# Optimization experiments

Hardware: AMD Instinct MI355X
Metric: run time of the kernel (lower is better)

Reference implementation:

```python
import jax, jax.numpy as jnp
import numpy as np

B, P, L, H = 64, 1024, 16, 256
NUM_SIZE = 18
TOPK = min(64, P)


def _ramp(epoch, a, b):
    if epoch <= a:
        return 0.0
    if epoch >= b:
        return 1.0
    return float(epoch - a) / float(b - a)


def _normalize(x):
    return x / jnp.maximum(jnp.linalg.norm(x, axis=-1, keepdims=True), 1e-12)


def setup_inputs() -> dict:
    key = jax.random.key(0)
    ks = jax.random.split(key, 16)
    return {
        'pred_center': jax.random.normal(ks[0], (B, P, 3), dtype=jnp.float32),
        'pred_size': jax.random.uniform(ks[1], (B, P, 3), minval=0.2, maxval=1.0, dtype=jnp.float32),
        'bbox_feature': jax.random.normal(ks[2], (B, P, H), dtype=jnp.float32),
        'objectness_scores': jax.random.normal(ks[3], (B, P, 2), dtype=jnp.float32),
        'lang_emb': jax.random.normal(ks[4], (B * L, H), dtype=jnp.float32),
        'lang_num': jax.random.randint(ks[5], (B,), 1, L + 1),
        'ref_center': jax.random.normal(ks[6], (B, L, 3), dtype=jnp.float32),
        'ref_size_class': jax.random.randint(ks[7], (B, L), 0, NUM_SIZE),
        'ref_size_residual': jax.random.uniform(ks[8], (B, L, 3), minval=0.0, maxval=0.2, dtype=jnp.float32),
        'mean_size_arr': jax.random.uniform(ks[9], (NUM_SIZE, 3), minval=0.3, maxval=1.5, dtype=jnp.float32),
        'W_text': jax.random.normal(ks[10], (H, H), dtype=jnp.float32) / np.sqrt(H),
        'W_pc': jax.random.normal(ks[11], (H, H), dtype=jnp.float32) / np.sqrt(H),
        'W_pc_iou': jax.random.normal(ks[12], (H, H), dtype=jnp.float32) / np.sqrt(H),
        'log_inv_tau': jnp.array([np.log(1.0 / 0.07)], dtype=jnp.float32),
        'epoch': 40,
    }


def _forward(pred_center, pred_size, bbox_feature, objectness_scores, lang_emb,
             lang_num, ref_center, ref_size_class, ref_size_residual,
             mean_size_arr, W_text, W_pc, W_pc_iou, log_inv_tau, epoch):
    b, l = ref_center.shape[:2]
    # curriculum (python scalars, epoch is a static int)
    p = _ramp(epoch, 0, 80)
    thr = 0.05 + 0.3 * p
    gamma = 1.0 + 2.0 * p
    min_tau = 0.08 - 0.04 * p

    # top-k proposals by objectness prob
    obj_prob = jax.nn.softmax(objectness_scores, axis=2)[..., 1]  # (B,P)
    _, topk_inds = jax.lax.top_k(obj_prob, TOPK)                  # (B,K)
    feat = jnp.take_along_axis(bbox_feature, topk_inds[..., None], axis=1)  # (B,K,H)
    ctr = jnp.take_along_axis(pred_center, topk_inds[..., None], axis=1)    # (B,K,3)
    sz = jnp.take_along_axis(pred_size, topk_inds[..., None], axis=1)       # (B,K,3)

    # axis-aligned 3D IoU between gt boxes (B,L) and pred boxes (B,K) -- detached
    gt_size = mean_size_arr[ref_size_class] + ref_size_residual + 0.01  # (B,L,3)
    gmin, gmax = ref_center - gt_size / 2, ref_center + gt_size / 2
    pmin, pmax = ctr - sz / 2, ctr + sz / 2
    lo = jnp.maximum(gmin[:, :, None], pmin[:, None])   # (B,L,K,3)
    hi = jnp.minimum(gmax[:, :, None], pmax[:, None])
    inter = jnp.prod(jnp.clip(hi - lo, 0.0, None), axis=-1)  # (B,L,K)
    vol_g = jnp.prod(gt_size, axis=-1)[:, :, None]
    vol_p = jnp.prod(sz, axis=-1)[:, None]
    iou = jax.lax.stop_gradient(inter / (vol_g + vol_p - inter + 1e-7))  # (B,L,K)

    # soft target over proposals (detached)
    w = jnp.clip(iou, 0.0, None) ** gamma * (iou >= thr).astype(iou.dtype)
    onehot = jax.nn.one_hot(jnp.argmax(iou, axis=-1), TOPK, dtype=iou.dtype)
    w = jnp.where(w.sum(-1, keepdims=True) < 1e-6, onehot, w)
    target = w / (w.sum(-1, keepdims=True) + 1e-6)  # (B,L,K)

    # temperature
    inv_tau = jnp.minimum(jnp.exp(log_inv_tau)[0], 100.0)
    inv_tau = jnp.minimum(inv_tau, 1.0 / max(min_tau, 1e-6))

    # language-box contrastive
    text = _normalize(lang_emb.reshape(b, l, -1) @ W_text.T)  # (B,L,H)
    boxf = _normalize(feat @ W_pc.T)                          # (B,K,H)
    sim = jnp.einsum('blh,bkh->blk', text, boxf)              # (B,L,K)
    logp = jax.nn.log_softmax(sim * inv_tau, axis=-1)
    t2 = target / (target.sum(-1, keepdims=True) + 1e-6)      # soft_ce renorm
    ce = -(t2 * logp).sum(-1)                                 # (B,L)

    neg = iou < 0.05
    s_neg = jnp.max(jnp.where(neg, sim, -jnp.inf), axis=-1)
    s_pos = (sim * target).sum(-1)
    rank = jnp.where(neg.any(-1), jax.nn.relu(0.2 - s_pos + s_neg), 0.0)
    lang_con = ce + 0.5 * rank                                # (B,L)

    mask = (jnp.arange(l)[None, :] < lang_num[:, None]).astype(sim.dtype)
    lang_loss = (lang_con * mask).sum() / b

    # iou-aware box-box contrastive
    tm = w[..., :, None] * w[..., None, :]                    # (B,L,K,K) detached
    tm = tm / (tm.sum(-1, keepdims=True) + 1e-6)
    tm = tm / (tm.sum(-1, keepdims=True) + 1e-6)              # soft_ce renorm
    boxf_iou = _normalize(feat @ W_pc_iou.T)                  # (B,K,H)
    sim_iou = jnp.einsum('bkh,bmh->bkm', boxf_iou, boxf_iou)  # (B,K,K)
    logp_iou = jax.nn.log_softmax(sim_iou * inv_tau, axis=-1)
    iou_ce = -(tm * logp_iou[:, None]).sum(-1).mean(-1)       # (B,L)
    iou_loss = (iou_ce * mask).sum() / b

    return jnp.stack([lang_loss, iou_loss])


def reference(pred_center, pred_size, bbox_feature, objectness_scores, lang_emb,
              lang_num, ref_center, ref_size_class, ref_size_residual,
              mean_size_arr, W_text, W_pc, W_pc_iou, log_inv_tau, epoch):
    return _forward(pred_center, pred_size, bbox_feature, objectness_scores,
                    lang_emb, lang_num, ref_center, ref_size_class,
                    ref_size_residual, mean_size_arr, W_text, W_pc, W_pc_iou,
                    log_inv_tau, epoch)
```

## Files before the change

kernel.cpp:

```cpp
#include <hip/hip_runtime.h>
#include <math.h>

#define B 64
#define P 1024
#define L 16
#define H 256
#define K 64

__device__ __forceinline__ float wsum(float v){
  #pragma unroll
  for (int o = 32; o >= 1; o >>= 1) v += __shfl_xor(v, o, 64);
  return v;
}
__device__ __forceinline__ float wmaxr(float v){
  #pragma unroll
  for (int o = 32; o >= 1; o >>= 1) v = fmaxf(v, __shfl_xor(v, o, 64));
  return v;
}
__device__ __forceinline__ void wargmax(float &v, int &i){
  #pragma unroll
  for (int o = 32; o >= 1; o >>= 1){
    float v2 = __shfl_xor(v, o, 64);
    int   i2 = __shfl_xor(i, o, 64);
    if (v2 > v || (v2 == v && i2 < i)){ v = v2; i = i2; }
  }
}
__device__ __forceinline__ unsigned fkey(float f){
  unsigned b = __float_as_uint(f);
  return (b & 0x80000000u) ? ~b : (b | 0x80000000u);
}
__device__ __forceinline__ float dot4(float4 a, float4 b){
  return a.x*b.x + a.y*b.y + a.z*b.z + a.w*b.w;
}
__device__ __forceinline__ int gsw(int r){ return (r ^ (r >> 3)) & 7; }

__global__ __launch_bounds__(256) void k_topk_iou(
    const float* __restrict__ pred_center, const float* __restrict__ pred_size,
    const float* __restrict__ obj, const float* __restrict__ ref_center,
    const int* __restrict__ ref_cls, const float* __restrict__ ref_res,
    const float* __restrict__ mean_sz, const int* __restrict__ epoch_p,
    const int* __restrict__ lang_num,
    int* __restrict__ inds, float* __restrict__ iou_ws, float* __restrict__ w_ws,
    float* __restrict__ c_ws, float* __restrict__ t_ws, float* __restrict__ t2_ws,
    float* __restrict__ t2s_ws, int* __restrict__ cnt)
{
  __shared__ int hist[256];
  __shared__ int s_digit, s_cum;
  __shared__ int waveTot[4];
  __shared__ int sel[K];
  __shared__ float ctrS[K][3], szS[K][3];
  int b = blockIdx.x, tid = threadIdx.x, lane = tid & 63, wave = tid >> 6;
  if (b == 0 && tid == 0) *cnt = 0;

  const float4* o4 = (const float4*)(obj + (size_t)b*P*2);
  float4 va = o4[tid*2], vb = o4[tid*2+1];
  unsigned kj[4] = { fkey(va.y - va.x), fkey(va.w - va.z),
                     fkey(vb.y - vb.x), fkey(vb.w - vb.z) };

  unsigned prefix = 0; int rem = K;
  for (int pass = 0; pass < 4; ++pass){
    int shift = 24 - pass*8;
    hist[tid] = 0;
    __syncthreads();
    #pragma unroll
    for (int j = 0; j < 4; ++j){
      unsigned kk = kj[j];
      bool cand = (pass == 0) || ((kk >> (shift + 8)) == prefix);
      if (cand) atomicAdd(&hist[(kk >> shift) & 0xff], 1);
    }
    __syncthreads();
    int d = 255 - tid;
    int h = hist[d];
    int s = h;
    #pragma unroll
    for (int o = 1; o < 64; o <<= 1){ int t = __shfl_up(s, o, 64); if (lane >= o) s += t; }
    if (lane == 63) waveTot[wave] = s;
    __syncthreads();
    #pragma unroll
    for (int q = 0; q < 3; ++q) if (q < wave) s += waveTot[q];
    if (s >= rem && s - h < rem){ s_digit = d; s_cum = s - h; }
    __syncthreads();
    prefix = (prefix << 8) | (unsigned)s_digit;
    rem -= s_cum;
    __syncthreads();
  }
  unsigned T = prefix;
  int remFinal = rem;

  int eqc = 0;
  #pragma unroll
  for (int j = 0; j < 4; ++j) eqc += (kj[j] == T) ? 1 : 0;
  int v = eqc;
  #pragma unroll
  for (int o = 1; o < 64; o <<= 1){ int t = __shfl_up(v, o, 64); if (lane >= o) v += t; }
  if (lane == 63) waveTot[wave] = v;
  __syncthreads();
  int off = 0;
  for (int q = 0; q < wave; ++q) off += waveTot[q];
  int e = off + v - eqc;
  __syncthreads();

  int selc = 0; bool ch[4];
  #pragma unroll
  for (int j = 0; j < 4; ++j){
    bool g = kj[j] > T;
    bool q = (kj[j] == T) && (e < remFinal);
    if (kj[j] == T) e++;
    ch[j] = g || q; selc += ch[j] ? 1 : 0;
  }
  v = selc;
  #pragma unroll
  for (int o = 1; o < 64; o <<= 1){ int t = __shfl_up(v, o, 64); if (lane >= o) v += t; }
  if (lane == 63) waveTot[wave] = v;
  __syncthreads();
  off = 0;
  for (int q = 0; q < wave; ++q) off += waveTot[q];
  int slot = off + v - selc;
  #pragma unroll
  for (int j = 0; j < 4; ++j) if (ch[j]) sel[slot++] = tid*4 + j;
  __syncthreads();

  if (tid < K){
    int idx = sel[tid];
    inds[b*K + tid] = idx;
    #pragma unroll
    for (int dd = 0; dd < 3; ++dd){
      ctrS[tid][dd] = pred_center[((size_t)b*P + idx)*3 + dd];
      szS [tid][dd] = pred_size [((size_t)b*P + idx)*3 + dd];
    }
  }
  __syncthreads();

  int ep = epoch_p[0];
  float pr = ep <= 0 ? 0.f : (ep >= 80 ? 1.f : ep / 80.f);
  float thr = 0.05f + 0.3f * pr;
  float gamma = 1.f + 2.f * pr;
  int ln = lang_num[b];

  for (int l = wave; l < L; l += 4){
    int cls = ref_cls[b*L + l];
    float gs[3], gc[3]; float volg = 1.f;
    #pragma unroll
    for (int dd = 0; dd < 3; ++dd){
      gs[dd] = mean_sz[cls*3+dd] + ref_res[((size_t)b*L+l)*3+dd] + 0.01f;
      gc[dd] = ref_center[((size_t)b*L+l)*3+dd];
      volg *= gs[dd];
    }
    int k = lane;
    float inter = 1.f, volp = 1.f;
    #pragma unroll
    for (int dd = 0; dd < 3; ++dd){
      float pc = ctrS[k][dd], ps = szS[k][dd];
      float lo = fmaxf(gc[dd]-gs[dd]*0.5f, pc-ps*0.5f);
      float hi = fminf(gc[dd]+gs[dd]*0.5f, pc+ps*0.5f);
      inter *= fmaxf(hi-lo, 0.f);
      volp *= ps;
    }
    float iou = inter / (volg + volp - inter + 1e-7f);
    float wv = (iou >= thr) ? powf(iou, gamma) : 0.f;
    float S = wsum(wv);
    float av = iou; int ai = k;
    wargmax(av, ai);
    float wfin = (S < 1e-6f) ? ((k == ai) ? 1.f : 0.f) : wv;
    iou_ws[((size_t)b*L + l)*K + k] = iou;
    w_ws  [((size_t)b*L + l)*K + k] = wfin;
    float Sf = (S < 1e-6f) ? 1.f : S;
    float a = wfin * Sf;
    float c = wfin / ((a + 1e-6f) * (a/(a + 1e-6f) + 1e-6f));
    c_ws[((size_t)b*L + l)*K + k] = (l < ln) ? c : 0.f;
    float target = wfin / (Sf + 1e-6f);
    float tsum = Sf / (Sf + 1e-6f);
    float t2 = target / (tsum + 1e-6f);
    t_ws [((size_t)b*L + l)*K + k] = target;
    t2_ws[((size_t)b*L + l)*K + k] = t2;
    float T2S = wsum(t2);
    if (lane == 0) t2s_ws[b*L + l] = T2S;
  }
}

__global__ __launch_bounds__(256) void k_gemm(
    const float* __restrict__ bbox_feature, const int* __restrict__ inds,
    const float* __restrict__ lang_emb,
    const float* __restrict__ Wpc, const float* __restrict__ Wpci,
    const float* __restrict__ Wtext,
    float* __restrict__ boxr, float* __restrict__ boxri, float* __restrict__ texr)
{
  __shared__ float As[2][32][68], Ws[2][32][68];
  int gb = blockIdx.x;
  const float *W; float *C; int m0; bool gat;
  if (gb < 64)       { W = Wpc;   C = boxr;  m0 = gb*64;       gat = true;  }
  else if (gb < 128) { W = Wpci;  C = boxri; m0 = (gb-64)*64;  gat = true;  }
  else               { W = Wtext; C = texr;  m0 = (gb-128)*64; gat = false; }
  int bcol = blockIdx.y * 64;
  int tid = threadIdx.x;
  int lr = tid >> 2, lc = (tid & 3) * 4;
  int tr = tid >> 4, tc = tid & 15;
  int r = m0 + lr;
  const float* Arow = gat ? bbox_feature + ((size_t)(r >> 6)*P + inds[r])*H
                          : lang_emb + (size_t)r*H;
  const float* Wrow = W + (size_t)(bcol + lr)*H;
  float acc[4][4] = {};

  {
    float4 av  = *(const float4*)&Arow[lc];
    float4 av2 = *(const float4*)&Arow[16 + lc];
    float4 wv  = *(const float4*)&Wrow[lc];
    float4 wv2 = *(const float4*)&Wrow[16 + lc];
    As[0][lc+0][lr]=av.x;  As[0][lc+1][lr]=av.y;  As[0][lc+2][lr]=av.z;  As[0][lc+3][lr]=av.w;
    As[0][16+lc+0][lr]=av2.x; As[0][16+lc+1][lr]=av2.y; As[0][16+lc+2][lr]=av2.z; As[0][16+lc+3][lr]=av2.w;
    Ws[0][lc+0][lr]=wv.x;  Ws[0][lc+1][lr]=wv.y;  Ws[0][lc+2][lr]=wv.z;  Ws[0][lc+3][lr]=wv.w;
    Ws[0][16+lc+0][lr]=wv2.x; Ws[0][16+lc+1][lr]=wv2.y; Ws[0][16+lc+2][lr]=wv2.z; Ws[0][16+lc+3][lr]=wv2.w;
  }
  __syncthreads();

  int cur = 0;
  for (int h0 = 0; h0 < H; h0 += 32){
    float4 av, av2, wv, wv2;
    bool pre = (h0 + 32 < H);
    if (pre){
      av  = *(const float4*)&Arow[h0 + 32 + lc];
      av2 = *(const float4*)&Arow[h0 + 48 + lc];
      wv  = *(const float4*)&Wrow[h0 + 32 + lc];
      wv2 = *(const float4*)&Wrow[h0 + 48 + lc];
    }
    #pragma unroll
    for (int h = 0; h < 32; ++h){
      float4 a = *(const float4*)&As[cur][h][tr*4];
      float4 w = *(const float4*)&Ws[cur][h][tc*4];
      float aa[4] = {a.x,a.y,a.z,a.w};
      float ww[4] = {w.x,w.y,w.z,w.w};
      #pragma unroll
      for (int i = 0; i < 4; ++i)
        #pragma unroll
        for (int j = 0; j < 4; ++j) acc[i][j] += aa[i]*ww[j];
    }
    if (pre){
      int nx = cur ^ 1;
      As[nx][lc+0][lr]=av.x;  As[nx][lc+1][lr]=av.y;  As[nx][lc+2][lr]=av.z;  As[nx][lc+3][lr]=av.w;
      As[nx][16+lc+0][lr]=av2.x; As[nx][16+lc+1][lr]=av2.y; As[nx][16+lc+2][lr]=av2.z; As[nx][16+lc+3][lr]=av2.w;
      Ws[nx][lc+0][lr]=wv.x;  Ws[nx][lc+1][lr]=wv.y;  Ws[nx][lc+2][lr]=wv.z;  Ws[nx][lc+3][lr]=wv.w;
      Ws[nx][16+lc+0][lr]=wv2.x; Ws[nx][16+lc+1][lr]=wv2.y; Ws[nx][16+lc+2][lr]=wv2.z; Ws[nx][16+lc+3][lr]=wv2.w;
      __syncthreads();
      cur = nx;
    }
  }
  #pragma unroll
  for (int i = 0; i < 4; ++i){
    float4 v = make_float4(acc[i][0],acc[i][1],acc[i][2],acc[i][3]);
    *(float4*)&C[(size_t)(m0+tr*4+i)*H + bcol + tc*4] = v;
  }
}

__global__ __launch_bounds__(512) void k_contrast(
    const float* __restrict__ texr, const float* __restrict__ boxr,
    const float* __restrict__ boxri,
    const float* __restrict__ iou_ws, const float* __restrict__ w_ws,
    const float* __restrict__ c_ws, const float* __restrict__ t_ws,
    const float* __restrict__ t2_ws, const float* __restrict__ t2s_ws,
    const int* __restrict__ lang_num, const float* __restrict__ log_inv_tau,
    const int* __restrict__ epoch_p, float* __restrict__ part,
    int* __restrict__ cnt, float* __restrict__ out)
{
  extern __shared__ __align__(16) float smem[];
  __shared__ float redI[8], redL[8];
  __shared__ int s_done;
  int tid = threadIdx.x, lane = tid & 63, wave = tid >> 6;
  int ep = epoch_p[0];
  float pr = ep <= 0 ? 0.f : (ep >= 80 ? 1.f : ep / 80.f);
  float min_tau = fmaxf(0.08f - 0.04f*pr, 1e-6f);
  float itau = fminf(fminf(expf(log_inv_tau[0]), 100.f), 1.f/min_tau);

  if (blockIdx.x < 64){
    int b = blockIdx.x;
    float4* TB = (float4*)smem;
    float4* TT = (float4*)smem + 4096;
    const float4* srcB = (const float4*)(boxr + (size_t)b*K*H);
    const float4* srcT = (const float4*)(texr + (size_t)b*L*H);
    #pragma unroll
    for (int j = 0; j < 8; ++j){
      int i4 = tid + 512*j;
      int row = i4 >> 6, c = i4 & 63;
      TB[row*64 + (c ^ gsw(row))] = srcB[i4];
    }
    #pragma unroll
    for (int j = 0; j < 2; ++j){
      int i4 = tid + 512*j;
      int row = i4 >> 6, c = i4 & 63;
      TT[row*64 + (c ^ gsw(row))] = srcT[i4];
    }
    __syncthreads();

    int l0 = wave*2;
    float acc[2] = {0,0}, nt2[2] = {0,0};
    float nb2 = 0.f;
    for (int c = 0; c < 64; ++c){
      float4 bx = TB[lane*64 + (c ^ gsw(lane))];
      nb2 += dot4(bx, bx);
      #pragma unroll
      for (int i = 0; i < 2; ++i){
        int l = l0 + i;
        float4 tv = TT[l*64 + (c ^ gsw(l))];
        acc[i] += dot4(tv, bx);
        nt2[i] += dot4(tv, tv);
      }
    }
    float nb = fmaxf(sqrtf(nb2), 1e-12f);
    int ln = lang_num[b];
    float bacc = 0.f;
    #pragma unroll
    for (int i = 0; i < 2; ++i){
      int l = l0 + i;
      if (l < ln){
        float sv = acc[i] / (fmaxf(sqrtf(nt2[i]), 1e-12f) * nb);
        float target = t_ws [((size_t)b*L + l)*K + lane];
        float t2     = t2_ws[((size_t)b*L + l)*K + lane];
        float iou    = iou_ws[((size_t)b*L + l)*K + lane];
        float T2S    = t2s_ws[b*L + l];
        float z = sv * itau;
        float zmax = wmaxr(z);
        float se = wsum(expf(z - zmax));
        float t2z = wsum(t2 * z);
        float ce = -t2z + (zmax + logf(se)) * T2S;
        bool neg = iou < 0.05f;
        float sneg = wmaxr(neg ? sv : -INFINITY);
        int anyneg = __any(neg);
        float spos = wsum(sv * target);
        float rank = anyneg ? fmaxf(0.2f - spos + sneg, 0.f) : 0.f;
        bacc += ce + 0.5f*rank;
      }
    }
    if (lane == 0) atomicExch(&part[blockIdx.x*8 + wave], bacc);
  } else {
    int idx = blockIdx.x - 64;
    int b = idx >> 1, half = idx & 1;
    int r0 = half*32 + wave*4;
    float4* TI = (float4*)smem;
    float*  cL = smem + 16384;
    const float4* srcI = (const float4*)(boxri + (size_t)b*K*H);
    #pragma unroll
    for (int j = 0; j < 8; ++j){
      int i4 = tid + 512*j;
      int row = i4 >> 6, c = i4 & 63;
      TI[row*64 + (c ^ gsw(row))] = srcI[i4];
    }
    {
      int l = tid >> 5, kk = tid & 31;
      cL[l*32 + kk] = c_ws[((size_t)b*L + l)*K + half*32 + kk];
    }
    float wl[16];
    #pragma unroll
    for (int l = 0; l < 16; ++l) wl[l] = w_ws[((size_t)b*L + l)*K + lane];
    __syncthreads();

    float acc[4] = {0,0,0,0};
    float nm2 = 0.f;
    for (int c = 0; c < 64; ++c){
      float4 bx = TI[lane*64 + (c ^ gsw(lane))];
      nm2 += dot4(bx, bx);
      #pragma unroll
      for (int i = 0; i < 4; ++i){
        float4 kq = TI[(r0+i)*64 + (c ^ gsw(r0+i))];
        acc[i] += dot4(kq, bx);
      }
    }
    float4 Mv = make_float4(0.f,0.f,0.f,0.f);
    #pragma unroll
    for (int l = 0; l < 16; ++l){
      float4 cq = *(const float4*)&cL[l*32 + wave*4];
      Mv.x += cq.x * wl[l]; Mv.y += cq.y * wl[l];
      Mv.z += cq.z * wl[l]; Mv.w += cq.w * wl[l];
    }
    float Ma[4] = {Mv.x, Mv.y, Mv.z, Mv.w};
    float nm = fmaxf(sqrtf(nm2), 1e-12f);
    float contrib = 0.f;
    #pragma unroll
    for (int i = 0; i < 4; ++i){
      float nk = __shfl(nm, r0 + i, 64);
      float sv = acc[i] / (nk * nm);
      float z = sv * itau;
      float zmax = wmaxr(z);
      float se = wsum(expf(z - zmax));
      float lp = z - zmax - logf(se);
      contrib += Ma[i] * lp;
    }
    float bacc = -wsum(contrib) * (1.f/64.f);
    if (lane == 0) atomicExch(&part[512 + idx*8 + wave], bacc);
  }

  __syncthreads();
  if (tid == 0){
    __threadfence();
    int t = atomicAdd(cnt, 1);
    s_done = (t == 191) ? 1 : 0;
  }
  __syncthreads();
  if (s_done){
    float vl = atomicAdd(&part[tid], 0.f);
    float vi = atomicAdd(&part[512 + tid], 0.f)
             + atomicAdd(&part[1024 + tid], 0.f);
    vi = wsum(vi);
    vl = wsum(vl);
    if (lane == 0){ redI[wave] = vi; redL[wave] = vl; }
    __syncthreads();
    if (tid == 0){
      float sl = 0.f, si = 0.f;
      #pragma unroll
      for (int q = 0; q < 8; ++q){ sl += redL[q]; si += redI[q]; }
      out[0] = sl * (1.f/64.f);
      out[1] = si * (1.f/64.f);
    }
  }
}

extern "C" void kernel_launch(void* const* d_in, const int* in_sizes, int n_in,
                              void* d_out, int out_size, void* d_ws, size_t ws_size,
                              hipStream_t stream)
{
  const float* pred_center = (const float*)d_in[0];
  const float* pred_size   = (const float*)d_in[1];
  const float* bbox_feature= (const float*)d_in[2];
  const float* obj         = (const float*)d_in[3];
  const float* lang_emb    = (const float*)d_in[4];
  const int*   lang_num    = (const int*)d_in[5];
  const float* ref_center  = (const float*)d_in[6];
  const int*   ref_cls     = (const int*)d_in[7];
  const float* ref_res     = (const float*)d_in[8];
  const float* mean_sz     = (const float*)d_in[9];
  const float* Wtext       = (const float*)d_in[10];
  const float* Wpc         = (const float*)d_in[11];
  const float* Wpci        = (const float*)d_in[12];
  const float* lit         = (const float*)d_in[13];
  const int*   epoch       = (const int*)d_in[14];

  float* ws = (float*)d_ws;
  int*   inds   = (int*)ws;
  float* iou_ws = ws + 4096;
  float* w_ws   = iou_ws + B*L*K;
  float* c_ws   = w_ws + B*L*K;
  float* t_ws   = c_ws + B*L*K;
  float* t2_ws  = t_ws + B*L*K;
  float* t2s_ws = t2_ws + B*L*K;
  float* texr   = t2s_ws + B*L;
  float* boxr   = texr + (size_t)B*L*H;
  float* boxri  = boxr + (size_t)B*K*H;
  float* part   = boxri + (size_t)B*K*H;
  int*   cnt    = (int*)(part + 1536);

  k_topk_iou<<<B, 256, 0, stream>>>(pred_center, pred_size, obj, ref_center,
                                    ref_cls, ref_res, mean_sz, epoch, lang_num,
                                    inds, iou_ws, w_ws, c_ws, t_ws, t2_ws, t2s_ws,
                                    cnt);
  k_gemm<<<dim3(144, 4), 256, 0, stream>>>(bbox_feature, inds, lang_emb,
                                           Wpc, Wpci, Wtext, boxr, boxri, texr);
  k_contrast<<<192, 512, 81920, stream>>>(texr, boxr, boxri,
                                          iou_ws, w_ws, c_ws, t_ws, t2_ws, t2s_ws,
                                          lang_num, lit, epoch, part, cnt,
                                          (float*)d_out);
}
```

Measured before the change: 58.90 us.

## Rewrite projection GEMM as one-wave blocks with 8x8 register tiles

The gather+projection GEMM is restructured so each 64-thread block computes a 64x64 output tile, with every thread holding an 8x8 accumulator instead of 4x4. The grid is flattened to 576 blocks, and the double-buffered shared-memory pipeline is replaced by a single buffer with two barriers per 32-wide K slice. The aim is more register-level reuse per shared-memory load, at the cost of fewer waves per block, higher register pressure and no overlap between global loads and compute.

```diff
diff --git a/kernel.cpp b/kernel.cpp
--- a/kernel.cpp
+++ b/kernel.cpp
@@ -178,76 +178,63 @@
   }
 }
 
-__global__ __launch_bounds__(256) void k_gemm(
+__global__ __launch_bounds__(64) void k_gemm(
     const float* __restrict__ bbox_feature, const int* __restrict__ inds,
     const float* __restrict__ lang_emb,
     const float* __restrict__ Wpc, const float* __restrict__ Wpci,
     const float* __restrict__ Wtext,
     float* __restrict__ boxr, float* __restrict__ boxri, float* __restrict__ texr)
 {
-  __shared__ float As[2][32][68], Ws[2][32][68];
+  __shared__ float As[32][68], Ws[32][68];
   int gb = blockIdx.x;
-  const float *W; float *C; int m0; bool gat;
-  if (gb < 64)       { W = Wpc;   C = boxr;  m0 = gb*64;       gat = true;  }
-  else if (gb < 128) { W = Wpci;  C = boxri; m0 = (gb-64)*64;  gat = true;  }
-  else               { W = Wtext; C = texr;  m0 = (gb-128)*64; gat = false; }
-  int bcol = blockIdx.y * 64;
+  const float *W; float *C; int m0, bcol; bool gat;
+  if (gb < 256)      { W = Wpc;   C = boxr;  m0 = (gb>>2)*64;       bcol = (gb&3)*64; gat = true;  }
+  else if (gb < 512) { W = Wpci;  C = boxri; m0 = ((gb-256)>>2)*64; bcol = (gb&3)*64; gat = true;  }
+  else               { W = Wtext; C = texr;  m0 = ((gb-512)>>2)*64; bcol = (gb&3)*64; gat = false; }
   int tid = threadIdx.x;
-  int lr = tid >> 2, lc = (tid & 3) * 4;
-  int tr = tid >> 4, tc = tid & 15;
-  int r = m0 + lr;
-  const float* Arow = gat ? bbox_feature + ((size_t)(r >> 6)*P + inds[r])*H
-                          : lang_emb + (size_t)r*H;
-  const float* Wrow = W + (size_t)(bcol + lr)*H;
-  float acc[4][4] = {};
-
-  {
-    float4 av  = *(const float4*)&Arow[lc];
-    float4 av2 = *(const float4*)&Arow[16 + lc];
-    float4 wv  = *(const float4*)&Wrow[lc];
-    float4 wv2 = *(const float4*)&Wrow[16 + lc];
-    As[0][lc+0][lr]=av.x;  As[0][lc+1][lr]=av.y;  As[0][lc+2][lr]=av.z;  As[0][lc+3][lr]=av.w;
-    As[0][16+lc+0][lr]=av2.x; As[0][16+lc+1][lr]=av2.y; As[0][16+lc+2][lr]=av2.z; As[0][16+lc+3][lr]=av2.w;
-    Ws[0][lc+0][lr]=wv.x;  Ws[0][lc+1][lr]=wv.y;  Ws[0][lc+2][lr]=wv.z;  Ws[0][lc+3][lr]=wv.w;
-    Ws[0][16+lc+0][lr]=wv2.x; Ws[0][16+lc+1][lr]=wv2.y; Ws[0][16+lc+2][lr]=wv2.z; Ws[0][16+lc+3][lr]=wv2.w;
-  }
-  __syncthreads();
-
-  int cur = 0;
-  for (int h0 = 0; h0 < H; h0 += 32){
-    float4 av, av2, wv, wv2;
-    bool pre = (h0 + 32 < H);
-    if (pre){
-      av  = *(const float4*)&Arow[h0 + 32 + lc];
-      av2 = *(const float4*)&Arow[h0 + 48 + lc];
-      wv  = *(const float4*)&Wrow[h0 + 32 + lc];
-      wv2 = *(const float4*)&Wrow[h0 + 48 + lc];
-    }
+  int tr = tid >> 3, tc = tid & 7;
+  int sr = tid >> 3, sc = tid & 7;
+
+  float acc[8][8] = {};
+  for (int h0 = 0; h0 < 64; h0 += 8){
+    #pragma unroll
+    for (int j = 0; j < 8; ++j){
+      int row = sr + 8*j;
+      int r = m0 + row;
+      const float4* asrc = gat
+        ? (const float4*)(bbox_feature + ((size_t)(r >> 6)*P + inds[r])*H)
+        : (const float4*)(lang_emb + (size_t)r*H);
+      const float4* wsrc = (const float4*)(W + (size_t)(bcol + row)*H);
+      float4 av = asrc[h0 + sc];
+      float4 wv = wsrc[h0 + sc];
+      As[sc*4+0][row] = av.x; As[sc*4+1][row] = av.y;
+      As[sc*4+2][row] = av.z; As[sc*4+3][row] = av.w;
+      Ws[sc*4+0][row] = wv.x; Ws[sc*4+1][row] = wv.y;
+      Ws[sc*4+2][row] = wv.z; Ws[sc*4+3][row] = wv.w;
+    }
+    __syncthreads();
     #pragma unroll
     for (int h = 0; h < 32; ++h){
-      float4 a = *(const float4*)&As[cur][h][tr*4];
-      float4 w = *(const float4*)&Ws[cur][h][tc*4];
-      float aa[4] = {a.x,a.y,a.z,a.w};
-      float ww[4] = {w.x,w.y,w.z,w.w};
+      float4 a0 = *(const float4*)&As[h][tr*8];
+      float4 a1 = *(const float4*)&As[h][tr*8+4];
+      float4 w0 = *(const float4*)&Ws[h][tc*8];
+      float4 w1 = *(const float4*)&Ws[h][tc*8+4];
+      float aa[8] = {a0.x,a0.y,a0.z,a0.w,a1.x,a1.y,a1.z,a1.w};
+      float ww[8] = {w0.x,w0.y,w0.z,w0.w,w1.x,w1.y,w1.z,w1.w};
       #pragma unroll
-      for (int i = 0; i < 4; ++i)
+      for (int i = 0; i < 8; ++i)
         #pragma unroll
-        for (int j = 0; j < 4; ++j) acc[i][j] += aa[i]*ww[j];
-    }
-    if (pre){
-      int nx = cur ^ 1;
-      As[nx][lc+0][lr]=av.x;  As[nx][lc+1][lr]=av.y;  As[nx][lc+2][lr]=av.z;  As[nx][lc+3][lr]=av.w;
-      As[nx][16+lc+0][lr]=av2.x; As[nx][16+lc+1][lr]=av2.y; As[nx][16+lc+2][lr]=av2.z; As[nx][16+lc+3][lr]=av2.w;
-      Ws[nx][lc+0][lr]=wv.x;  Ws[nx][lc+1][lr]=wv.y;  Ws[nx][lc+2][lr]=wv.z;  Ws[nx][lc+3][lr]=wv.w;
-      Ws[nx][16+lc+0][lr]=wv2.x; Ws[nx][16+lc+1][lr]=wv2.y; Ws[nx][16+lc+2][lr]=wv2.z; Ws[nx][16+lc+3][lr]=wv2.w;
-      __syncthreads();
-      cur = nx;
-    }
-  }
-  #pragma unroll
-  for (int i = 0; i < 4; ++i){
-    float4 v = make_float4(acc[i][0],acc[i][1],acc[i][2],acc[i][3]);
-    *(float4*)&C[(size_t)(m0+tr*4+i)*H + bcol + tc*4] = v;
+        for (int j = 0; j < 8; ++j) acc[i][j] += aa[i]*ww[j];
+    }
+    __syncthreads();
+  }
+  #pragma unroll
+  for (int i = 0; i < 8; ++i){
+    float4 v0 = make_float4(acc[i][0],acc[i][1],acc[i][2],acc[i][3]);
+    float4 v1 = make_float4(acc[i][4],acc[i][5],acc[i][6],acc[i][7]);
+    size_t base = (size_t)(m0 + tr*8 + i)*H + bcol + tc*8;
+    *(float4*)&C[base]     = v0;
+    *(float4*)&C[base + 4] = v1;
   }
 }
 
@@ -450,8 +437,8 @@
                                     ref_cls, ref_res, mean_sz, epoch, lang_num,
                                     inds, iou_ws, w_ws, c_ws, t_ws, t2_ws, t2s_ws,
                                     cnt);
-  k_gemm<<<dim3(144, 4), 256, 0, stream>>>(bbox_feature, inds, lang_emb,
-                                           Wpc, Wpci, Wtext, boxr, boxri, texr);
+  k_gemm<<<dim3(576), 64, 0, stream>>>(bbox_feature, inds, lang_emb,
+                                       Wpc, Wpci, Wtext, boxr, boxri, texr);
   k_contrast<<<192, 512, 81920, stream>>>(texr, boxr, boxri,
                                           iou_ws, w_ws, c_ws, t_ws, t2_ws, t2s_ws,
                                           lang_num, lit, epoch, part, cnt,
```

New measurement: 88.31 us. +49.9%, slower.

## Split GEMM reduction dimension in two and sum partials in contrast kernel

Applied to the files above, without the earlier changes.

The GEMM grid gains a z dimension that splits the H=256 reduction into two halves. Each half writes its own partial output buffer, and the contrast kernel adds the two partials while loading them into shared memory. This doubles the GEMM block count (576 to 1152) to fill more compute units, and drops the register double-buffered prefetch in favour of a simpler single shared buffer. The cost is extra workspace, twice the partial-output writes, extra reads in the contrast kernel, and loads that no longer overlap with compute.

```diff
diff --git a/kernel.cpp b/kernel.cpp
--- a/kernel.cpp
+++ b/kernel.cpp
@@ -31,6 +31,9 @@
 }
 __device__ __forceinline__ float dot4(float4 a, float4 b){
   return a.x*b.x + a.y*b.y + a.z*b.z + a.w*b.w;
+}
+__device__ __forceinline__ float4 f4add(float4 a, float4 b){
+  return make_float4(a.x+b.x, a.y+b.y, a.z+b.z, a.w+b.w);
 }
 __device__ __forceinline__ int gsw(int r){ return (r ^ (r >> 3)) & 7; }
 
@@ -183,14 +186,16 @@
     const float* __restrict__ lang_emb,
     const float* __restrict__ Wpc, const float* __restrict__ Wpci,
     const float* __restrict__ Wtext,
-    float* __restrict__ boxr, float* __restrict__ boxri, float* __restrict__ texr)
+    float* __restrict__ boxr0, float* __restrict__ boxri0, float* __restrict__ texr0,
+    float* __restrict__ boxr1, float* __restrict__ boxri1, float* __restrict__ texr1)
 {
-  __shared__ float As[2][32][68], Ws[2][32][68];
+  __shared__ float As[32][68], Ws[32][68];
   int gb = blockIdx.x;
+  int z  = blockIdx.z;
   const float *W; float *C; int m0; bool gat;
-  if (gb < 64)       { W = Wpc;   C = boxr;  m0 = gb*64;       gat = true;  }
-  else if (gb < 128) { W = Wpci;  C = boxri; m0 = (gb-64)*64;  gat = true;  }
-  else               { W = Wtext; C = texr;  m0 = (gb-128)*64; gat = false; }
+  if (gb < 64)       { W = Wpc;   C = z ? boxr1  : boxr0;  m0 = gb*64;       gat = true;  }
+  else if (gb < 128) { W = Wpci;  C = z ? boxri1 : boxri0; m0 = (gb-64)*64;  gat = true;  }
+  else               { W = Wtext; C = z ? texr1  : texr0;  m0 = (gb-128)*64; gat = false; }
   int bcol = blockIdx.y * 64;
   int tid = threadIdx.x;
   int lr = tid >> 2, lc = (tid & 3) * 4;
@@ -200,33 +205,21 @@
                           : lang_emb + (size_t)r*H;
   const float* Wrow = W + (size_t)(bcol + lr)*H;
   float acc[4][4] = {};
-
-  {
-    float4 av  = *(const float4*)&Arow[lc];
-    float4 av2 = *(const float4*)&Arow[16 + lc];
-    float4 wv  = *(const float4*)&Wrow[lc];
-    float4 wv2 = *(const float4*)&Wrow[16 + lc];
-    As[0][lc+0][lr]=av.x;  As[0][lc+1][lr]=av.y;  As[0][lc+2][lr]=av.z;  As[0][lc+3][lr]=av.w;
-    As[0][16+lc+0][lr]=av2.x; As[0][16+lc+1][lr]=av2.y; As[0][16+lc+2][lr]=av2.z; As[0][16+lc+3][lr]=av2.w;
-    Ws[0][lc+0][lr]=wv.x;  Ws[0][lc+1][lr]=wv.y;  Ws[0][lc+2][lr]=wv.z;  Ws[0][lc+3][lr]=wv.w;
-    Ws[0][16+lc+0][lr]=wv2.x; Ws[0][16+lc+1][lr]=wv2.y; Ws[0][16+lc+2][lr]=wv2.z; Ws[0][16+lc+3][lr]=wv2.w;
-  }
-  __syncthreads();
-
-  int cur = 0;
-  for (int h0 = 0; h0 < H; h0 += 32){
-    float4 av, av2, wv, wv2;
-    bool pre = (h0 + 32 < H);
-    if (pre){
-      av  = *(const float4*)&Arow[h0 + 32 + lc];
-      av2 = *(const float4*)&Arow[h0 + 48 + lc];
-      wv  = *(const float4*)&Wrow[h0 + 32 + lc];
-      wv2 = *(const float4*)&Wrow[h0 + 48 + lc];
-    }
+  int hbeg = z * 128, hend = hbeg + 128;
+  for (int h0 = hbeg; h0 < hend; h0 += 32){
+    float4 av  = *(const float4*)&Arow[h0 + lc];
+    float4 av2 = *(const float4*)&Arow[h0 + 16 + lc];
+    float4 wv  = *(const float4*)&Wrow[h0 + lc];
+    float4 wv2 = *(const float4*)&Wrow[h0 + 16 + lc];
+    As[lc+0][lr]=av.x;  As[lc+1][lr]=av.y;  As[lc+2][lr]=av.z;  As[lc+3][lr]=av.w;
+    As[16+lc+0][lr]=av2.x; As[16+lc+1][lr]=av2.y; As[16+lc+2][lr]=av2.z; As[16+lc+3][lr]=av2.w;
+    Ws[lc+0][lr]=wv.x;  Ws[lc+1][lr]=wv.y;  Ws[lc+2][lr]=wv.z;  Ws[lc+3][lr]=wv.w;
+    Ws[16+lc+0][lr]=wv2.x; Ws[16+lc+1][lr]=wv2.y; Ws[16+lc+2][lr]=wv2.z; Ws[16+lc+3][lr]=wv2.w;
+    __syncthreads();
     #pragma unroll
     for (int h = 0; h < 32; ++h){
-      float4 a = *(const float4*)&As[cur][h][tr*4];
-      float4 w = *(const float4*)&Ws[cur][h][tc*4];
+      float4 a = *(const float4*)&As[h][tr*4];
+      float4 w = *(const float4*)&Ws[h][tc*4];
       float aa[4] = {a.x,a.y,a.z,a.w};
       float ww[4] = {w.x,w.y,w.z,w.w};
       #pragma unroll
@@ -234,15 +227,7 @@
         #pragma unroll
         for (int j = 0; j < 4; ++j) acc[i][j] += aa[i]*ww[j];
     }
-    if (pre){
-      int nx = cur ^ 1;
-      As[nx][lc+0][lr]=av.x;  As[nx][lc+1][lr]=av.y;  As[nx][lc+2][lr]=av.z;  As[nx][lc+3][lr]=av.w;
-      As[nx][16+lc+0][lr]=av2.x; As[nx][16+lc+1][lr]=av2.y; As[nx][16+lc+2][lr]=av2.z; As[nx][16+lc+3][lr]=av2.w;
-      Ws[nx][lc+0][lr]=wv.x;  Ws[nx][lc+1][lr]=wv.y;  Ws[nx][lc+2][lr]=wv.z;  Ws[nx][lc+3][lr]=wv.w;
-      Ws[nx][16+lc+0][lr]=wv2.x; Ws[nx][16+lc+1][lr]=wv2.y; Ws[nx][16+lc+2][lr]=wv2.z; Ws[nx][16+lc+3][lr]=wv2.w;
-      __syncthreads();
-      cur = nx;
-    }
+    __syncthreads();
   }
   #pragma unroll
   for (int i = 0; i < 4; ++i){
@@ -252,8 +237,9 @@
 }
 
 __global__ __launch_bounds__(512) void k_contrast(
-    const float* __restrict__ texr, const float* __restrict__ boxr,
-    const float* __restrict__ boxri,
+    const float* __restrict__ texr0, const float* __restrict__ texr1,
+    const float* __restrict__ boxr0, const float* __restrict__ boxr1,
+    const float* __restrict__ boxri0, const float* __restrict__ boxri1,
     const float* __restrict__ iou_ws, const float* __restrict__ w_ws,
     const float* __restrict__ c_ws, const float* __restrict__ t_ws,
     const float* __restrict__ t2_ws, const float* __restrict__ t2s_ws,
@@ -274,19 +260,21 @@
     int b = blockIdx.x;
     float4* TB = (float4*)smem;
     float4* TT = (float4*)smem + 4096;
-    const float4* srcB = (const float4*)(boxr + (size_t)b*K*H);
-    const float4* srcT = (const float4*)(texr + (size_t)b*L*H);
+    const float4* srcB0 = (const float4*)(boxr0 + (size_t)b*K*H);
+    const float4* srcB1 = (const float4*)(boxr1 + (size_t)b*K*H);
+    const float4* srcT0 = (const float4*)(texr0 + (size_t)b*L*H);
+    const float4* srcT1 = (const float4*)(texr1 + (size_t)b*L*H);
     #pragma unroll
     for (int j = 0; j < 8; ++j){
       int i4 = tid + 512*j;
       int row = i4 >> 6, c = i4 & 63;
-      TB[row*64 + (c ^ gsw(row))] = srcB[i4];
+      TB[row*64 + (c ^ gsw(row))] = f4add(srcB0[i4], srcB1[i4]);
     }
     #pragma unroll
     for (int j = 0; j < 2; ++j){
       int i4 = tid + 512*j;
       int row = i4 >> 6, c = i4 & 63;
-      TT[row*64 + (c ^ gsw(row))] = srcT[i4];
+      TT[row*64 + (c ^ gsw(row))] = f4add(srcT0[i4], srcT1[i4]);
     }
     __syncthreads();
 
@@ -336,12 +324,13 @@
     int r0 = half*32 + wave*4;
     float4* TI = (float4*)smem;
     float*  cL = smem + 16384;
-    const float4* srcI = (const float4*)(boxri + (size_t)b*K*H);
+    const float4* srcI0 = (const float4*)(boxri0 + (size_t)b*K*H);
+    const float4* srcI1 = (const float4*)(boxri1 + (size_t)b*K*H);
     #pragma unroll
     for (int j = 0; j < 8; ++j){
       int i4 = tid + 512*j;
       int row = i4 >> 6, c = i4 & 63;
-      TI[row*64 + (c ^ gsw(row))] = srcI[i4];
+      TI[row*64 + (c ^ gsw(row))] = f4add(srcI0[i4], srcI1[i4]);
     }
     {
       int l = tid >> 5, kk = tid & 31;
@@ -440,19 +429,25 @@
   float* t_ws   = c_ws + B*L*K;
   float* t2_ws  = t_ws + B*L*K;
   float* t2s_ws = t2_ws + B*L*K;
-  float* texr   = t2s_ws + B*L;
-  float* boxr   = texr + (size_t)B*L*H;
-  float* boxri  = boxr + (size_t)B*K*H;
-  float* part   = boxri + (size_t)B*K*H;
+  float* texr0  = t2s_ws + B*L;
+  float* texr1  = texr0 + (size_t)B*L*H;
+  float* boxr0  = texr1 + (size_t)B*L*H;
+  float* boxr1  = boxr0 + (size_t)B*K*H;
+  float* boxri0 = boxr1 + (size_t)B*K*H;
+  float* boxri1 = boxri0 + (size_t)B*K*H;
+  float* part   = boxri1 + (size_t)B*K*H;
   int*   cnt    = (int*)(part + 1536);
 
   k_topk_iou<<<B, 256, 0, stream>>>(pred_center, pred_size, obj, ref_center,
                                     ref_cls, ref_res, mean_sz, epoch, lang_num,
                                     inds, iou_ws, w_ws, c_ws, t_ws, t2_ws, t2s_ws,
                                     cnt);
-  k_gemm<<<dim3(144, 4), 256, 0, stream>>>(bbox_feature, inds, lang_emb,
-                                           Wpc, Wpci, Wtext, boxr, boxri, texr);
-  k_contrast<<<192, 512, 81920, stream>>>(texr, boxr, boxri,
+  k_gemm<<<dim3(144, 4, 2), 256, 0, stream>>>(bbox_feature, inds, lang_emb,
+                                              Wpc, Wpci, Wtext,
+                                              boxr0, boxri0, texr0,
+                                              boxr1, boxri1, texr1);
+  k_contrast<<<192, 512, 81920, stream>>>(texr0, texr1, boxr0, boxr1,
+                                          boxri0, boxri1,
                                           iou_ws, w_ws, c_ws, t_ws, t2_ws, t2s_ws,
                                           lang_num, lit, epoch, part, cnt,
                                           (float*)d_out);
```

Result: no change. 58.44 us (-0.8%).
